# Optimization experiments

Hardware: AMD Instinct MI355X
Metric: run time of the kernel (lower is better)

## Reference

```python
import jax, jax.numpy as jnp
import numpy as np

RMS_EPS = 1e-8
Q_EPS = 1e-5

def rms_norm(x):
    # RMSNorm without learnable scale, as in BitNet reference BitLinear
    return x * jax.lax.rsqrt(jnp.mean(x * x, axis=-1, keepdims=True) + RMS_EPS)

def activation_quant(x):
    # per-token absmax int8 quant/dequant
    scale = 127.0 / jnp.clip(jnp.max(jnp.abs(x), axis=-1, keepdims=True), Q_EPS)
    return jnp.clip(jnp.round(x * scale), -128, 127) / scale

def weight_quant(w):
    # ternary absmean quant/dequant
    scale = 1.0 / jnp.clip(jnp.mean(jnp.abs(w)), Q_EPS)
    return jnp.clip(jnp.round(w * scale), -1, 1) / scale

def bitlinear(x, w):
    # forward path of BitLinear: RMSNorm -> quantized matmul (STE is identity in fwd)
    xn = rms_norm(x)
    xq = xn + jax.lax.stop_gradient(activation_quant(xn) - xn)
    wq = w + jax.lax.stop_gradient(weight_quant(w) - w)
    return jnp.einsum('bsh,oh->bso', xq, wq)

def setup_inputs() -> dict:
    key = jax.random.key(0)
    k1, k2, k3 = jax.random.split(key, 3)
    H, I = 2048, 8192  # hidden_size, intermediate_size = 4*H
    x = jax.random.normal(k1, (4, 2048, H), jnp.float32)
    w_gate = jax.random.normal(k2, (2 * I, H), jnp.float32) * 0.02
    w_down = jax.random.normal(k3, (H, I), jnp.float32) * 0.02
    return {"x": x, "w_gate": w_gate, "w_down": w_down}

def reference(x, w_gate, w_down):
    y = bitlinear(x, w_gate)          # [B,S,2I]
    gate, v = jnp.split(y, 2, axis=-1)
    return bitlinear(jax.nn.silu(gate) * v, w_down)  # [B,S,H]
```

## Files before the change

### kernel.cpp

```cpp
#include <hip/hip_runtime.h>


using char8  = __attribute__((ext_vector_type(8))) signed char;
using int4v  = __attribute__((ext_vector_type(4))) int;
using half8  = __attribute__((ext_vector_type(8))) _Float16;

__device__ __forceinline__ void glds16(const void* g, void* l) {
  __builtin_amdgcn_global_load_lds((const __attribute__((address_space(1))) void*)g,
                                   (__attribute__((address_space(3))) void*)l, 16, 0, 0);
}

__global__ __launch_bounds__(256) void reduce_abs_kernel(
    const float4* __restrict__ w, float* __restrict__ partials, int n4) {
  int t = threadIdx.x;
  int gid = blockIdx.x * 256 + t;
  int stride = gridDim.x * 256;
  float s = 0.f;
  for (int i = gid; i < n4; i += stride) {
    float4 u = w[i];
    s += fabsf(u.x) + fabsf(u.y) + fabsf(u.z) + fabsf(u.w);
  }
  __shared__ float sm[256];
  sm[t] = s; __syncthreads();
  for (int off = 128; off > 0; off >>= 1) {
    if (t < off) sm[t] += sm[t + off];
    __syncthreads();
  }
  if (t == 0) partials[blockIdx.x] = sm[0];
}

__global__ __launch_bounds__(256) void finalize_kernel(
    const float* __restrict__ pf, float* __restrict__ scales) {
  __shared__ float sm[256];
  int t = threadIdx.x;
  float s = pf[t] + pf[t + 256] + pf[t + 512] + pf[t + 768];
  sm[t] = s; __syncthreads();
  for (int off = 128; off > 0; off >>= 1) {
    if (t < off) sm[t] += sm[t + off];
    __syncthreads();
  }
  if (t == 0) {
    float c = fmaxf(sm[0] / 33554432.0f, 1e-5f);
    scales[0] = c; scales[2] = 1.0f / c;
  }
  __syncthreads();
  s = pf[1024 + t] + pf[1280 + t] + pf[1536 + t] + pf[1792 + t];
  sm[t] = s; __syncthreads();
  for (int off = 128; off > 0; off >>= 1) {
    if (t < off) sm[t] += sm[t + off];
    __syncthreads();
  }
  if (t == 0) {
    float c = fmaxf(sm[0] / 16777216.0f, 1e-5f);
    scales[1] = c; scales[3] = 1.0f / c;
  }
}

__global__ __launch_bounds__(256) void quant_weight_kernel(
    const float4* __restrict__ w, char8* __restrict__ wq,
    const float* __restrict__ invp, int n8) {
  float inv = *invp;
  int stride = gridDim.x * 256;
  for (int i = blockIdx.x * 256 + threadIdx.x; i < n8; i += stride) {
    float4 a = w[2 * i], b = w[2 * i + 1];
    float v[8] = {a.x, a.y, a.z, a.w, b.x, b.y, b.z, b.w};
    char8 o;
#pragma unroll
    for (int j = 0; j < 8; ++j) {
      float q = rintf(v[j] * inv);
      q = fminf(fmaxf(q, -1.f), 1.f);
      o[j] = (signed char)(int)q;
    }
    wq[i] = o;
  }
}

__global__ __launch_bounds__(256) void act_quant_f32_kernel(
    const float* __restrict__ in, signed char* __restrict__ out,
    float* __restrict__ fscale) {
  const int token = blockIdx.x, t = threadIdx.x;
  const float4* row = (const float4*)(in + (size_t)token * 2048);
  float4 a = row[2 * t], b = row[2 * t + 1];
  float v[8] = {a.x, a.y, a.z, a.w, b.x, b.y, b.z, b.w};
  float ss = 0.f, am = 0.f;
#pragma unroll
  for (int j = 0; j < 8; ++j) { ss += v[j] * v[j]; am = fmaxf(am, fabsf(v[j])); }
  __shared__ float s1[256], s2[256];
  s1[t] = ss; s2[t] = am; __syncthreads();
  for (int off = 128; off > 0; off >>= 1) {
    if (t < off) { s1[t] += s1[t + off]; s2[t] = fmaxf(s2[t], s2[t + off]); }
    __syncthreads();
  }
  float r = 1.0f / sqrtf(s1[0] * (1.0f / 2048.0f) + 1e-8f);
  float f = fmaxf(s2[0] * r, 1e-5f);
  float s = 127.0f / f;
  if (t == 0) fscale[token] = f * (1.0f / 127.0f);
  char8 o;
#pragma unroll
  for (int j = 0; j < 8; ++j) {
    float q = rintf((v[j] * r) * s);
    q = fminf(fmaxf(q, -128.f), 127.f);
    o[j] = (signed char)(int)q;
  }
  ((char8*)(out + (size_t)token * 2048))[t] = o;
}

__global__ __launch_bounds__(256) void act_quant_h_kernel(
    const _Float16* __restrict__ in, signed char* __restrict__ out,
    float* __restrict__ fscale) {
  const int token = blockIdx.x, t = threadIdx.x;
  const half8* row = (const half8*)(in + (size_t)token * 8192);
  float v[32];
  float ss = 0.f, am = 0.f;
#pragma unroll
  for (int c = 0; c < 4; ++c) {
    half8 u = row[c * 256 + t];
#pragma unroll
    for (int j = 0; j < 8; ++j) {
      float f = (float)u[j]; v[c * 8 + j] = f;
      ss += f * f; am = fmaxf(am, fabsf(f));
    }
  }
  __shared__ float s1[256], s2[256];
  s1[t] = ss; s2[t] = am; __syncthreads();
  for (int off = 128; off > 0; off >>= 1) {
    if (t < off) { s1[t] += s1[t + off]; s2[t] = fmaxf(s2[t], s2[t + off]); }
    __syncthreads();
  }
  float r = 1.0f / sqrtf(s1[0] * (1.0f / 8192.0f) + 1e-8f);
  float f = fmaxf(s2[0] * r, 1e-5f);
  float s = 127.0f / f;
  if (t == 0) fscale[token] = f * (1.0f / 127.0f);
#pragma unroll
  for (int c = 0; c < 4; ++c) {
    char8 o;
#pragma unroll
    for (int j = 0; j < 8; ++j) {
      float q = rintf((v[c * 8 + j] * r) * s);
      q = fminf(fmaxf(q, -128.f), 127.f);
      o[j] = (signed char)(int)q;
    }
    ((char8*)(out + (size_t)token * 8192))[c * 256 + t] = o;
  }
}

__global__ __launch_bounds__(256, 2) void gemm1_kernel(
    const signed char* __restrict__ A,
    const signed char* __restrict__ B,
    const float* __restrict__ f1, const float* __restrict__ cgp,
    _Float16* __restrict__ Z) {
  constexpr int K = 2048, I = 8192, NT = K / 64;
  constexpr int BUF = 24576;
  __shared__ __align__(16) signed char Ls[2 * BUF];
  const int t0 = blockIdx.y * 128, n0 = blockIdx.x * 128;
  const int tid = threadIdx.x, w = tid >> 6, l = tid & 63;
  const int wm = (w >> 1) * 64, wn = (w & 1) * 64;
  const int lrow = l & 15, lchunk = (l >> 4) * 16;

  int4v ag[4][4], av[4][4];
#pragma unroll
  for (int i = 0; i < 4; ++i)
#pragma unroll
    for (int j = 0; j < 4; ++j) { ag[i][j] = {0,0,0,0}; av[i][j] = {0,0,0,0}; }

  const signed char* src[6];
  int dst[6];
#pragma unroll
  for (int r = 0; r < 6; ++r) {
    int u = w * 6 + r;
    if (u < 8) {
      src[r] = A + (size_t)(t0 + u * 16 + lrow) * K + lchunk;
      dst[r] = u * 1024;
    } else {
      int v = u - 8;
      int grow = (v < 8) ? (n0 + v * 16 + lrow) : (I + n0 + (v - 8) * 16 + lrow);
      src[r] = B + (size_t)grow * K + lchunk;
      dst[r] = 8192 + v * 1024;
    }
  }

#pragma unroll
  for (int r = 0; r < 6; ++r) glds16(src[r], &Ls[dst[r]]);
  __syncthreads();

  const int aoff = (wm >> 4) * 1024 + l * 16;
  const int goff = 8192 + (wn >> 4) * 1024 + l * 16;
  const int voff = goff + 8 * 1024;

#pragma unroll 2
  for (int it = 0; it < NT; ++it) {
    const int cur = (it & 1) * BUF;
    const int nxt = BUF - cur;
    if (it + 1 < NT) {
      const int ko = (it + 1) * 64;
#pragma unroll
      for (int r = 0; r < 6; ++r) glds16(src[r] + ko, &Ls[nxt + dst[r]]);
    }
    int4v af[4], bg[4], bv[4];
#pragma unroll
    for (int i = 0; i < 4; ++i) af[i] = *(const int4v*)&Ls[cur + aoff + i * 1024];
#pragma unroll
    for (int j = 0; j < 4; ++j) {
      bg[j] = *(const int4v*)&Ls[cur + goff + j * 1024];
      bv[j] = *(const int4v*)&Ls[cur + voff + j * 1024];
    }
#pragma unroll
    for (int i = 0; i < 4; ++i)
#pragma unroll
      for (int j = 0; j < 4; ++j) {
        ag[i][j] = __builtin_amdgcn_mfma_i32_16x16x64_i8(af[i], bg[j], ag[i][j], 0, 0, 0);
        av[i][j] = __builtin_amdgcn_mfma_i32_16x16x64_i8(af[i], bv[j], av[i][j], 0, 0, 0);
      }
    __syncthreads();
  }

  float cg = *cgp;
#pragma unroll
  for (int i = 0; i < 4; ++i)
#pragma unroll
    for (int rr = 0; rr < 4; ++rr) {
      int m = wm + i * 16 + (l >> 4) * 4 + rr;
      float fs = f1[t0 + m] * cg;
#pragma unroll
      for (int j = 0; j < 4; ++j) {
        int n = wn + j * 16 + (l & 15);
        float g = (float)ag[i][j][rr] * fs, vv = (float)av[i][j][rr] * fs;
        float z = g / (1.0f + __expf(-g)) * vv;
        Z[(size_t)(t0 + m) * I + n0 + n] = (_Float16)z;
      }
    }
}

__global__ __launch_bounds__(256, 2) void gemm2_kernel(
    const signed char* __restrict__ A,
    const signed char* __restrict__ B,
    const float* __restrict__ f2, const float* __restrict__ cdp,
    float* __restrict__ out) {
  constexpr int K = 8192, N = 2048, NT = K / 64;
  constexpr int BUF = 24576;
  __shared__ __align__(16) signed char Ls[2 * BUF];
  const int t0 = blockIdx.y * 128, n0 = blockIdx.x * 256;
  const int tid = threadIdx.x, w = tid >> 6, l = tid & 63;
  const int wm = (w >> 1) * 64, wn = (w & 1) * 128;
  const int lrow = l & 15, lchunk = (l >> 4) * 16;

  int4v acc[4][8];
#pragma unroll
  for (int i = 0; i < 4; ++i)
#pragma unroll
    for (int j = 0; j < 8; ++j) acc[i][j] = {0,0,0,0};

  const signed char* src[6];
  int dst[6];
#pragma unroll
  for (int r = 0; r < 6; ++r) {
    int u = w * 6 + r;
    if (u < 8) {
      src[r] = A + (size_t)(t0 + u * 16 + lrow) * K + lchunk;
      dst[r] = u * 1024;
    } else {
      int v = u - 8;
      src[r] = B + (size_t)(n0 + v * 16 + lrow) * K + lchunk;
      dst[r] = 8192 + v * 1024;
    }
  }

#pragma unroll
  for (int r = 0; r < 6; ++r) glds16(src[r], &Ls[dst[r]]);
  __syncthreads();

  const int aoff = (wm >> 4) * 1024 + l * 16;
  const int boff = 8192 + (wn >> 4) * 1024 + l * 16;

#pragma unroll 2
  for (int it = 0; it < NT; ++it) {
    const int cur = (it & 1) * BUF;
    const int nxt = BUF - cur;
    if (it + 1 < NT) {
      const int ko = (it + 1) * 64;
#pragma unroll
      for (int r = 0; r < 6; ++r) glds16(src[r] + ko, &Ls[nxt + dst[r]]);
    }
    int4v af[4], bf[8];
#pragma unroll
    for (int i = 0; i < 4; ++i) af[i] = *(const int4v*)&Ls[cur + aoff + i * 1024];
#pragma unroll
    for (int j = 0; j < 8; ++j) bf[j] = *(const int4v*)&Ls[cur + boff + j * 1024];
#pragma unroll
    for (int i = 0; i < 4; ++i)
#pragma unroll
      for (int j = 0; j < 8; ++j)
        acc[i][j] = __builtin_amdgcn_mfma_i32_16x16x64_i8(af[i], bf[j], acc[i][j], 0, 0, 0);
    __syncthreads();
  }

  float cd = *cdp;
#pragma unroll
  for (int i = 0; i < 4; ++i)
#pragma unroll
    for (int rr = 0; rr < 4; ++rr) {
      int m = wm + i * 16 + (l >> 4) * 4 + rr;
      float fs = f2[t0 + m] * cd;
#pragma unroll
      for (int j = 0; j < 8; ++j) {
        int n = wn + j * 16 + (l & 15);
        out[(size_t)(t0 + m) * N + n0 + n] = (float)acc[i][j][rr] * fs;
      }
    }
}

extern "C" void kernel_launch(void* const* d_in, const int* in_sizes, int n_in,
                              void* d_out, int out_size, void* d_ws, size_t ws_size,
                              hipStream_t stream) {
  const float* x  = (const float*)d_in[0];
  const float* wg = (const float*)d_in[1];
  const float* wd = (const float*)d_in[2];
  float* out = (float*)d_out;

  char* ws = (char*)d_ws;
  signed char* wgq = (signed char*)(ws);
  signed char* wdq = (signed char*)(ws + 33554432);
  signed char* xq  = (signed char*)(ws + 50331648);
  signed char* zq  = (signed char*)(ws + 67108864);
  _Float16*    z   = (_Float16*)  (ws + 134217728);
  float* f1     = (float*)(ws + 268435456);
  float* f2     = (float*)(ws + 268468224);
  float* pf     = (float*)(ws + 268500992);
  float* scales = (float*)(ws + 268509184);

  reduce_abs_kernel<<<1024, 256, 0, stream>>>((const float4*)wg, pf, 8388608);
  reduce_abs_kernel<<<1024, 256, 0, stream>>>((const float4*)wd, pf + 1024, 4194304);
  finalize_kernel<<<1, 256, 0, stream>>>(pf, scales);

  quant_weight_kernel<<<2048, 256, 0, stream>>>((const float4*)wg, (char8*)wgq, scales + 2, 4194304);
  quant_weight_kernel<<<1024, 256, 0, stream>>>((const float4*)wd, (char8*)wdq, scales + 3, 2097152);
  act_quant_f32_kernel<<<8192, 256, 0, stream>>>(x, xq, f1);

  gemm1_kernel<<<dim3(64, 64), 256, 0, stream>>>(xq, wgq, f1, scales, z);

  act_quant_h_kernel<<<8192, 256, 0, stream>>>(z, zq, f2);

  gemm2_kernel<<<dim3(8, 64), 256, 0, stream>>>(zq, wdq, f2, scales + 1, out);
}
```

Baseline: 932.6 us.

## Triple-buffer LDS in both int8 GEMMs with explicit vmcnt waits and setprio

Both GEMM kernels now use three LDS stages instead of two and prefetch two tiles ahead. The __syncthreads calls are replaced by raw s_barrier plus fine-grained s_waitcnt vmcnt counts, so only the oldest tile load has to finish before compute. MFMA sections are wrapped in s_setprio to favour matrix issue. The aim is to hide global-load latency better. In exchange LDS use per block grows to 72KB, which may limit the two blocks per CU assumed by launch_bounds, and the hand-counted vmcnt values are fragile if the compiler adds other memory operations.

```diff
diff --git a/kernel.cpp b/kernel.cpp
--- a/kernel.cpp
+++ b/kernel.cpp
@@ -151,7 +151,7 @@
     _Float16* __restrict__ Z) {
   constexpr int K = 2048, I = 8192, NT = K / 64;
   constexpr int BUF = 24576;
-  __shared__ __align__(16) signed char Ls[2 * BUF];
+  __shared__ __align__(16) signed char Ls[3 * BUF];
   const int t0 = blockIdx.y * 128, n0 = blockIdx.x * 128;
   const int tid = threadIdx.x, w = tid >> 6, l = tid & 63;
   const int wm = (w >> 1) * 64, wn = (w & 1) * 64;
@@ -180,30 +180,28 @@
   }
 
 #pragma unroll
-  for (int r = 0; r < 6; ++r) glds16(src[r], &Ls[dst[r]]);
-  __syncthreads();
+  for (int p = 0; p < 3; ++p)
+#pragma unroll
+    for (int r = 0; r < 6; ++r) glds16(src[r] + p * 64, &Ls[p * BUF + dst[r]]);
+  asm volatile("s_waitcnt vmcnt(12)" ::: "memory");
+  __builtin_amdgcn_s_barrier();
+  __builtin_amdgcn_sched_barrier(0);
 
   const int aoff = (wm >> 4) * 1024 + l * 16;
   const int goff = 8192 + (wn >> 4) * 1024 + l * 16;
   const int voff = goff + 8 * 1024;
 
-#pragma unroll 2
+  int curo = 0;
   for (int it = 0; it < NT; ++it) {
-    const int cur = (it & 1) * BUF;
-    const int nxt = BUF - cur;
-    if (it + 1 < NT) {
-      const int ko = (it + 1) * 64;
-#pragma unroll
-      for (int r = 0; r < 6; ++r) glds16(src[r] + ko, &Ls[nxt + dst[r]]);
-    }
     int4v af[4], bg[4], bv[4];
 #pragma unroll
-    for (int i = 0; i < 4; ++i) af[i] = *(const int4v*)&Ls[cur + aoff + i * 1024];
+    for (int i = 0; i < 4; ++i) af[i] = *(const int4v*)&Ls[curo + aoff + i * 1024];
 #pragma unroll
     for (int j = 0; j < 4; ++j) {
-      bg[j] = *(const int4v*)&Ls[cur + goff + j * 1024];
-      bv[j] = *(const int4v*)&Ls[cur + voff + j * 1024];
-    }
+      bg[j] = *(const int4v*)&Ls[curo + goff + j * 1024];
+      bv[j] = *(const int4v*)&Ls[curo + voff + j * 1024];
+    }
+    __builtin_amdgcn_s_setprio(1);
 #pragma unroll
     for (int i = 0; i < 4; ++i)
 #pragma unroll
@@ -211,7 +209,21 @@
         ag[i][j] = __builtin_amdgcn_mfma_i32_16x16x64_i8(af[i], bg[j], ag[i][j], 0, 0, 0);
         av[i][j] = __builtin_amdgcn_mfma_i32_16x16x64_i8(af[i], bv[j], av[i][j], 0, 0, 0);
       }
-    __syncthreads();
+    __builtin_amdgcn_s_setprio(0);
+    if (it + 3 < NT) {
+      __builtin_amdgcn_s_barrier();
+      __builtin_amdgcn_sched_barrier(0);
+#pragma unroll
+      for (int r = 0; r < 6; ++r) glds16(src[r] + (it + 3) * 64, &Ls[curo + dst[r]]);
+    }
+    if (it < NT - 3)        asm volatile("s_waitcnt vmcnt(12)" ::: "memory");
+    else if (it == NT - 3)  asm volatile("s_waitcnt vmcnt(6)" ::: "memory");
+    else if (it == NT - 2)  asm volatile("s_waitcnt vmcnt(0)" ::: "memory");
+    if (it + 1 < NT) {
+      __builtin_amdgcn_s_barrier();
+      __builtin_amdgcn_sched_barrier(0);
+    }
+    curo += BUF; if (curo == 3 * BUF) curo = 0;
   }
 
   float cg = *cgp;
@@ -238,7 +250,7 @@
     float* __restrict__ out) {
   constexpr int K = 8192, N = 2048, NT = K / 64;
   constexpr int BUF = 24576;
-  __shared__ __align__(16) signed char Ls[2 * BUF];
+  __shared__ __align__(16) signed char Ls[3 * BUF];
   const int t0 = blockIdx.y * 128, n0 = blockIdx.x * 256;
   const int tid = threadIdx.x, w = tid >> 6, l = tid & 63;
   const int wm = (w >> 1) * 64, wn = (w & 1) * 128;
@@ -266,32 +278,44 @@
   }
 
 #pragma unroll
-  for (int r = 0; r < 6; ++r) glds16(src[r], &Ls[dst[r]]);
-  __syncthreads();
+  for (int p = 0; p < 3; ++p)
+#pragma unroll
+    for (int r = 0; r < 6; ++r) glds16(src[r] + p * 64, &Ls[p * BUF + dst[r]]);
+  asm volatile("s_waitcnt vmcnt(12)" ::: "memory");
+  __builtin_amdgcn_s_barrier();
+  __builtin_amdgcn_sched_barrier(0);
 
   const int aoff = (wm >> 4) * 1024 + l * 16;
   const int boff = 8192 + (wn >> 4) * 1024 + l * 16;
 
-#pragma unroll 2
+  int curo = 0;
   for (int it = 0; it < NT; ++it) {
-    const int cur = (it & 1) * BUF;
-    const int nxt = BUF - cur;
-    if (it + 1 < NT) {
-      const int ko = (it + 1) * 64;
-#pragma unroll
-      for (int r = 0; r < 6; ++r) glds16(src[r] + ko, &Ls[nxt + dst[r]]);
-    }
     int4v af[4], bf[8];
 #pragma unroll
-    for (int i = 0; i < 4; ++i) af[i] = *(const int4v*)&Ls[cur + aoff + i * 1024];
-#pragma unroll
-    for (int j = 0; j < 8; ++j) bf[j] = *(const int4v*)&Ls[cur + boff + j * 1024];
+    for (int i = 0; i < 4; ++i) af[i] = *(const int4v*)&Ls[curo + aoff + i * 1024];
+#pragma unroll
+    for (int j = 0; j < 8; ++j) bf[j] = *(const int4v*)&Ls[curo + boff + j * 1024];
+    __builtin_amdgcn_s_setprio(1);
 #pragma unroll
     for (int i = 0; i < 4; ++i)
 #pragma unroll
       for (int j = 0; j < 8; ++j)
         acc[i][j] = __builtin_amdgcn_mfma_i32_16x16x64_i8(af[i], bf[j], acc[i][j], 0, 0, 0);
-    __syncthreads();
+    __builtin_amdgcn_s_setprio(0);
+    if (it + 3 < NT) {
+      __builtin_amdgcn_s_barrier();
+      __builtin_amdgcn_sched_barrier(0);
+#pragma unroll
+      for (int r = 0; r < 6; ++r) glds16(src[r] + (it + 3) * 64, &Ls[curo + dst[r]]);
+    }
+    if (it < NT - 3)        asm volatile("s_waitcnt vmcnt(12)" ::: "memory");
+    else if (it == NT - 3)  asm volatile("s_waitcnt vmcnt(6)" ::: "memory");
+    else if (it == NT - 2)  asm volatile("s_waitcnt vmcnt(0)" ::: "memory");
+    if (it + 1 < NT) {
+      __builtin_amdgcn_s_barrier();
+      __builtin_amdgcn_sched_barrier(0);
+    }
+    curo += BUF; if (curo == 3 * BUF) curo = 0;
   }
 
   float cd = *cdp;
```

After: 911.1 us. 2.3% less time.
